# Optimization experiments

Measured on AMD Instinct MI355X. Metric: run time of the kernel, lower is better.

## Reference

```python
import jax, jax.numpy as jnp
import numpy as np

NUM_SKILLS = 1000
DIM_S = 64
SIZE_M = 64
B, T = 64, 200


def setup_inputs() -> dict:
    key = jax.random.key(0)
    ks = jax.random.split(key, 16)
    skills = jax.random.randint(ks[0], (B, T), 0, NUM_SKILLS)
    responses = jax.random.randint(ks[1], (B, T), 0, 2)
    s = 1.0 / np.sqrt(DIM_S)
    return {
        "skills": skills,
        "responses": responses,
        "k_emb": jax.random.normal(ks[2], (NUM_SKILLS, DIM_S)) * s,
        "v_emb": jax.random.normal(ks[3], (2 * NUM_SKILLS, DIM_S)) * s,
        "Mk": jax.random.normal(ks[4], (SIZE_M, DIM_S)) * np.sqrt(2.0 / DIM_S),
        "Mv0": jax.random.normal(ks[5], (SIZE_M, DIM_S)) * np.sqrt(2.0 / DIM_S),
        "fW": jax.random.normal(ks[6], (DIM_S, 2 * DIM_S)) * (1.0 / np.sqrt(2 * DIM_S)),
        "fb": jnp.zeros((DIM_S,)),
        "eW": jax.random.normal(ks[7], (DIM_S, DIM_S)) * s,
        "eb": jnp.zeros((DIM_S,)),
        "aW": jax.random.normal(ks[8], (DIM_S, DIM_S)) * s,
        "ab": jnp.zeros((DIM_S,)),
        "pW": jax.random.normal(ks[9], (1, DIM_S)) * s,
        "pb": jnp.zeros((1,)),
    }


def reference(skills, responses, k_emb, v_emb, Mk, Mv0, fW, fb, eW, eb, aW, ab, pW, pb):
    # dropout is identity in eval mode
    masked_r = responses * (responses > -1).astype(responses.dtype)
    x = skills + NUM_SKILLS * masked_r            # [B, T]
    k = k_emb[skills]                              # [B, T, D]
    v = v_emb[x]                                   # [B, T, D]
    w = jax.nn.softmax(jnp.einsum('btd,md->btm', k, Mk), axis=-1)  # [B, T, M]
    e = jax.nn.sigmoid(v @ eW.T + eb)              # [B, T, D]
    a = jnp.tanh(v @ aW.T + ab)                    # [B, T, D]

    Mv_init = jnp.broadcast_to(Mv0, (skills.shape[0],) + Mv0.shape)  # [B, M, D]

    def step(Mvt, inp):
        wt, et, at = inp                           # [B,M], [B,D], [B,D]
        read = jnp.einsum('bm,bmd->bd', wt, Mvt)   # read BEFORE update (Mv[:, :-1])
        Mvt = Mvt * (1.0 - wt[:, :, None] * et[:, None, :]) + wt[:, :, None] * at[:, None, :]
        return Mvt, read

    xs = (jnp.swapaxes(w, 0, 1), jnp.swapaxes(e, 0, 1), jnp.swapaxes(a, 0, 1))
    _, reads = jax.lax.scan(step, Mv_init, xs)     # reads: [T, B, D]
    reads = jnp.swapaxes(reads, 0, 1)              # [B, T, D]

    f = jnp.tanh(jnp.concatenate([reads, k], axis=-1) @ fW.T + fb)  # [B, T, D]
    p = jax.nn.sigmoid(f @ pW.T + pb)[..., 0]      # [B, T]
    return p[:, 1:]                                # pred, [B, T-1]
```

## Files before the change

### kernel.cpp

```cpp
#include <hip/hip_runtime.h>
#include <stdint.h>

#define NSK 1000
#define TT  200
#define BB  64
#define NROW (BB * TT)
#define NOUT (BB * (TT-1))
#define SCH 10
#define RW  2
#define NSPLIT 8
#define PSTR ((size_t)NROW * 64)

__device__ __forceinline__ unsigned ulane_bcast(unsigned v, int l) {
  return __builtin_amdgcn_readlane(v, l);
}
__device__ __forceinline__ float frcp(float x) { return __builtin_amdgcn_rcpf(x); }
__device__ __forceinline__ float sigm(float x) { return frcp(1.f + __expf(-x)); }
__device__ __forceinline__ float tanh_fast(float x) {
  return fmaf(-2.f, frcp(1.f + __expf(2.f * x)), 1.f);
}

typedef _Float16 half2v __attribute__((ext_vector_type(2)));
typedef _Float16 v8h __attribute__((ext_vector_type(8)));
typedef float    v4f __attribute__((ext_vector_type(4)));
union H2U { unsigned u; half2v h; };
union V8U { uint4 u; v8h h; };
__device__ __forceinline__ unsigned pack2h(float a, float b) {
  H2U x; x.h = (half2v){(_Float16)a, (_Float16)b}; return x.u;
}
__device__ __forceinline__ unsigned short f16bits(float x) {
  H2U u; u.h = (half2v){(_Float16)x, (_Float16)0.f}; return (unsigned short)(u.u & 0xffffu);
}
__device__ __forceinline__ float f16lo(unsigned bits) {
  H2U u; u.u = bits; return (float)u.h.x;
}
__device__ __forceinline__ float f16hi(unsigned bits) {
  H2U u; u.u = bits; return (float)u.h.y;
}
__device__ __forceinline__ v8h pk8(float4 x0, float4 x1) {
  return (v8h){(_Float16)x0.x, (_Float16)x0.y, (_Float16)x0.z, (_Float16)x0.w,
               (_Float16)x1.x, (_Float16)x1.y, (_Float16)x1.z, (_Float16)x1.w};
}

__global__ __launch_bounds__(256) void wea_scan(
    const int* __restrict__ skills, const int* __restrict__ responses,
    const float* __restrict__ k_emb, const float* __restrict__ v_emb,
    const float* __restrict__ Mk, const float* __restrict__ eW,
    const float* __restrict__ eb, const float* __restrict__ aW,
    const float* __restrict__ ab, const float* __restrict__ Mv0,
    unsigned short* __restrict__ pbase)
{
  __shared__ unsigned ea_lds[TT * 64];
  __shared__ unsigned short w_lds[TT * 8];
  __shared__ float red[2][SCH * 256];

  const int tid  = threadIdx.x;
  const int wv   = tid >> 6, lane = tid & 63;
  const int b    = blockIdx.x >> 3, s = blockIdx.x & 7;
  const int lr   = lane & 15;
  const int lg   = lane >> 4;
  const int cw   = s >> 1, lrh = s & 1;

  {
    float ebv[4], abv[4];
    #pragma unroll
    for (int c = 0; c < 4; ++c) { ebv[c] = eb[16 * c + lr]; abv[c] = ab[16 * c + lr]; }

    #pragma unroll 1
    for (int t = wv; t < 13; t += 4) {
      const int rbase = t * 16;
      const int rl    = min(rbase + lr, TT - 1);
      const int row   = b * TT + rl;
      const int sk = skills[row];
      int rr = responses[row]; rr = (rr > -1) ? rr : 0;
      const float4* kq = (const float4*)(k_emb + (size_t)sk * 64);
      const float4* vq = (const float4*)(v_emb + (size_t)(sk + NSK * rr) * 64);
      v8h ak[2], av[2];
      #pragma unroll
      for (int u = 0; u < 2; ++u) {
        const int o = u * 8 + lg * 2;
        ak[u] = pk8(kq[o], kq[o + 1]);
        av[u] = pk8(vq[o], vq[o + 1]);
      }

      v4f acK[4], acE[4], acA[4];
      #pragma unroll
      for (int c = 0; c < 4; ++c) {
        acK[c] = (v4f){0.f, 0.f, 0.f, 0.f};
        acE[c] = (v4f){0.f, 0.f, 0.f, 0.f};
        acA[c] = (v4f){0.f, 0.f, 0.f, 0.f};
      }
      #pragma unroll
      for (int c = 0; c < 4; ++c) {
        const float4* mq = (const float4*)(Mk + (size_t)(16 * c + lr) * 64);
        const float4* eq = (const float4*)(eW + (size_t)(16 * c + lr) * 64);
        const float4* aq = (const float4*)(aW + (size_t)(16 * c + lr) * 64);
        #pragma unroll
        for (int u = 0; u < 2; ++u) {
          const int o = u * 8 + lg * 2;
          const v8h bm = pk8(mq[o], mq[o + 1]);
          const v8h be = pk8(eq[o], eq[o + 1]);
          const v8h ba = pk8(aq[o], aq[o + 1]);
          acK[c] = __builtin_amdgcn_mfma_f32_16x16x32_f16(ak[u], bm, acK[c], 0, 0, 0);
          acE[c] = __builtin_amdgcn_mfma_f32_16x16x32_f16(av[u], be, acE[c], 0, 0, 0);
          acA[c] = __builtin_amdgcn_mfma_f32_16x16x32_f16(av[u], ba, acA[c], 0, 0, 0);
        }
      }

      float rs[4];
      #pragma unroll
      for (int q = 0; q < 4; ++q) {
        float m = fmaxf(fmaxf(acK[0][q], acK[1][q]), fmaxf(acK[2][q], acK[3][q]));
        #pragma unroll
        for (int off = 8; off; off >>= 1) m = fmaxf(m, __shfl_xor(m, off));
        float sm = 0.f;
        #pragma unroll
        for (int c = 0; c < 4; ++c) {
          acK[c][q] = __expf(acK[c][q] - m);
          sm += acK[c][q];
        }
        #pragma unroll
        for (int off = 8; off; off >>= 1) sm += __shfl_xor(sm, off);
        rs[q] = frcp(sm);
      }

      #pragma unroll
      for (int c = 0; c < 4; ++c) {
        const int j = 16 * c + lr;
        #pragma unroll
        for (int q = 0; q < 4; ++q) {
          const int rloc = rbase + lg * 4 + q;
          if (rloc < TT) {
            const float ev  = sigm(acE[c][q] + ebv[c]);
            const float avv = tanh_fast(acA[c][q] + abv[c]);
            ea_lds[rloc * 64 + j] = pack2h(ev, avv);
            if (c == cw && (lr >> 3) == lrh)
              w_lds[rloc * 8 + (lr & 7)] = f16bits(acK[c][q] * rs[q]);
          }
        }
      }
    }
  }
  __syncthreads();

  {
    const int m0 = s * 8 + wv * RW;
    unsigned short* ps = pbase + (size_t)s * PSTR;
    const size_t base = (size_t)b * TT;
    float Mv[RW];
    #pragma unroll
    for (int i = 0; i < RW; ++i) Mv[i] = Mv0[(size_t)(m0 + i) * 64 + lane];

    #pragma unroll 1
    for (int ch = 0; ch < TT / SCH; ++ch) {
      const int t0 = ch * SCH;
      float* rbuf = red[ch & 1];
      unsigned eab[SCH], wvb[SCH];
      #pragma unroll
      for (int k = 0; k < SCH; ++k) {
        eab[k] = ea_lds[(t0 + k) * 64 + lane];
        wvb[k] = (unsigned)w_lds[(t0 + k) * 8 + wv * RW + (lane & (RW - 1))];
      }
      #pragma unroll
      for (int k = 0; k < SCH; ++k) {
        const float ev = f16lo(eab[k]), av = f16hi(eab[k]);
        float rp = 0.f;
        #pragma unroll
        for (int i = 0; i < RW; ++i) {
          const float wm = f16lo(ulane_bcast(wvb[k], i));
          rp = fmaf(wm, Mv[i], rp);
          float tp = fmaf(-ev, Mv[i], av);
          Mv[i] = fmaf(wm, tp, Mv[i]);
        }
        rbuf[k * 256 + wv * 64 + lane] = rp;
      }
      __syncthreads();
      for (int k = wv; k < SCH; k += 4) {
        const float* rr2 = rbuf + k * 256;
        const float v = (rr2[lane] + rr2[64 + lane]) + (rr2[128 + lane] + rr2[192 + lane]);
        ps[(base + t0 + k) * 64 + lane] = f16bits(v);
      }
    }
  }
}

__global__ __launch_bounds__(256) void fp_mfma(
    const int* __restrict__ skills, const float* __restrict__ k_emb,
    const float* __restrict__ fW, const float* __restrict__ fb,
    const float* __restrict__ pW, const float* __restrict__ pb,
    const unsigned short* __restrict__ pbase,
    float* __restrict__ out)
{
  const int tid  = threadIdx.x;
  const int wv   = tid >> 6, lane = tid & 63;
  const int lr   = lane & 15;
  const int lg   = lane >> 4;
  const int o0   = (blockIdx.x * 4 + wv) * 16;

  const unsigned idx = o0 + lr;
  const unsigned bb  = idx / 199u;
  const unsigned t2  = idx - bb * 199u;
  const int srow     = (int)(idx + bb + 1u);

  v8h ar[4];
  #pragma unroll
  for (int t = 0; t < 2; ++t) {
    const size_t eo = (size_t)srow * 64 + t * 32 + lg * 8;
    V8U s0, s1, s2, s3;
    s0.u = *(const uint4*)&pbase[eo];
    s1.u = *(const uint4*)&pbase[eo + PSTR];
    s2.u = *(const uint4*)&pbase[eo + 2 * PSTR];
    s3.u = *(const uint4*)&pbase[eo + 3 * PSTR];
    v8h acc = (s0.h + s1.h) + (s2.h + s3.h);
    s0.u = *(const uint4*)&pbase[eo + 4 * PSTR];
    s1.u = *(const uint4*)&pbase[eo + 5 * PSTR];
    s2.u = *(const uint4*)&pbase[eo + 6 * PSTR];
    s3.u = *(const uint4*)&pbase[eo + 7 * PSTR];
    ar[t] = acc + ((s0.h + s1.h) + (s2.h + s3.h));
  }
  {
    const float4* kq = (const float4*)(k_emb + (size_t)skills[srow] * 64);
    #pragma unroll
    for (int t = 2; t < 4; ++t) {
      const int o = (t - 2) * 8 + lg * 2;
      ar[t] = pk8(kq[o], kq[o + 1]);
    }
  }

  float fbv[4], pwv[4];
  #pragma unroll
  for (int c = 0; c < 4; ++c) { fbv[c] = fb[16 * c + lr]; pwv[c] = pW[16 * c + lr]; }

  v4f acc[4];
  #pragma unroll
  for (int c = 0; c < 4; ++c) acc[c] = (v4f){0.f, 0.f, 0.f, 0.f};

  const float4* fq = (const float4*)fW;
  #pragma unroll
  for (int c = 0; c < 4; ++c) {
    const int jb = (16 * c + lr) * 32;
    #pragma unroll
    for (int t = 0; t < 4; ++t) {
      const int o = jb + t * 8 + lg * 2;
      const v8h bf = pk8(fq[o], fq[o + 1]);
      acc[c] = __builtin_amdgcn_mfma_f32_16x16x32_f16(ar[t], bf, acc[c], 0, 0, 0);
    }
  }

  const float pb0 = pb[0];
  #pragma unroll
  for (int q = 0; q < 4; ++q) {
    float s = 0.f;
    #pragma unroll
    for (int c = 0; c < 4; ++c)
      s += tanh_fast(acc[c][q] + fbv[c]) * pwv[c];
    #pragma unroll
    for (int off = 8; off; off >>= 1) s += __shfl_xor(s, off);
    if (lr == lg * 4 + q)
      out[(size_t)bb * (TT - 1) + t2] = sigm(s + pb0);
  }
}

extern "C" void kernel_launch(void* const* d_in, const int* in_sizes, int n_in,
                              void* d_out, int out_size, void* d_ws, size_t ws_size,
                              hipStream_t stream) {
  const int* skills    = (const int*)d_in[0];
  const int* responses = (const int*)d_in[1];
  const float* k_emb   = (const float*)d_in[2];
  const float* v_emb   = (const float*)d_in[3];
  const float* Mk      = (const float*)d_in[4];
  const float* Mv0     = (const float*)d_in[5];
  const float* fW      = (const float*)d_in[6];
  const float* fb      = (const float*)d_in[7];
  const float* eW      = (const float*)d_in[8];
  const float* eb      = (const float*)d_in[9];
  const float* aW      = (const float*)d_in[10];
  const float* ab      = (const float*)d_in[11];
  const float* pW      = (const float*)d_in[12];
  const float* pb      = (const float*)d_in[13];
  (void)in_sizes; (void)n_in; (void)out_size; (void)ws_size;

  unsigned short* pbase = (unsigned short*)d_ws;

  wea_scan<<<dim3(BB * NSPLIT), 256, 0, stream>>>(
      skills, responses, k_emb, v_emb, Mk, eW, eb, aW, ab, Mv0, pbase);
  fp_mfma<<<dim3(199), 256, 0, stream>>>(
      skills, k_emb, fW, fb, pW, pb, pbase, (float*)d_out);
}
```

Before: 132.2 us.

## Split scan across D columns instead of memory slots, removing partial-read reduction

Each of the 8 blocks per batch now owns 8 of the 64 D columns and all 64 memory slots, instead of 8 memory slots and all columns. The e/a projection therefore only computes its 16-column slice, and the read reduction over slots is done in-block with shuffles and a small LDS buffer. Each block writes final reads directly, so the second kernel no longer sums 8 fp16 partial buffers. The cost is shuffles every timestep and full 64-slot softmax weights kept in LDS; the scan chunk size also goes from 10 to 20.

Measured after the change: 137.1 us. +3.7%, slower.

```diff
diff --git a/kernel.cpp b/kernel.cpp
--- a/kernel.cpp
+++ b/kernel.cpp
@@ -5,15 +5,8 @@
 #define TT  200
 #define BB  64
 #define NROW (BB * TT)
-#define NOUT (BB * (TT-1))
-#define SCH 10
-#define RW  2
-#define NSPLIT 8
-#define PSTR ((size_t)NROW * 64)
-
-__device__ __forceinline__ unsigned ulane_bcast(unsigned v, int l) {
-  return __builtin_amdgcn_readlane(v, l);
-}
+#define SCH 20
+
 __device__ __forceinline__ float frcp(float x) { return __builtin_amdgcn_rcpf(x); }
 __device__ __forceinline__ float sigm(float x) { return frcp(1.f + __expf(-x)); }
 __device__ __forceinline__ float tanh_fast(float x) {
@@ -42,30 +35,27 @@
                (_Float16)x1.x, (_Float16)x1.y, (_Float16)x1.z, (_Float16)x1.w};
 }
 
-__global__ __launch_bounds__(256) void wea_scan(
+__global__ __launch_bounds__(256) void wea_scan_d(
     const int* __restrict__ skills, const int* __restrict__ responses,
     const float* __restrict__ k_emb, const float* __restrict__ v_emb,
     const float* __restrict__ Mk, const float* __restrict__ eW,
     const float* __restrict__ eb, const float* __restrict__ aW,
     const float* __restrict__ ab, const float* __restrict__ Mv0,
-    unsigned short* __restrict__ pbase)
+    unsigned short* __restrict__ reads_ws)
 {
-  __shared__ unsigned ea_lds[TT * 64];
-  __shared__ unsigned short w_lds[TT * 8];
-  __shared__ float red[2][SCH * 256];
+  __shared__ unsigned short w_lds[TT * 68];
+  __shared__ unsigned ea9[TT * 9];
+  __shared__ float red[2][SCH * 33];
 
   const int tid  = threadIdx.x;
   const int wv   = tid >> 6, lane = tid & 63;
-  const int b    = blockIdx.x >> 3, s = blockIdx.x & 7;
+  const int b    = blockIdx.x >> 3, q = blockIdx.x & 7;
+  const int cq   = q >> 1, h = q & 1;
   const int lr   = lane & 15;
   const int lg   = lane >> 4;
-  const int cw   = s >> 1, lrh = s & 1;
 
   {
-    float ebv[4], abv[4];
-    #pragma unroll
-    for (int c = 0; c < 4; ++c) { ebv[c] = eb[16 * c + lr]; abv[c] = ab[16 * c + lr]; }
-
+    const float ebl = eb[16 * cq + lr], abl = ab[16 * cq + lr];
     #pragma unroll 1
     for (int t = wv; t < 13; t += 4) {
       const int rbase = t * 16;
@@ -83,59 +73,63 @@
         av[u] = pk8(vq[o], vq[o + 1]);
       }
 
-      v4f acK[4], acE[4], acA[4];
-      #pragma unroll
-      for (int c = 0; c < 4; ++c) {
-        acK[c] = (v4f){0.f, 0.f, 0.f, 0.f};
-        acE[c] = (v4f){0.f, 0.f, 0.f, 0.f};
-        acA[c] = (v4f){0.f, 0.f, 0.f, 0.f};
-      }
+      v4f acK[4], acE, acA;
+      #pragma unroll
+      for (int c = 0; c < 4; ++c) acK[c] = (v4f){0.f, 0.f, 0.f, 0.f};
+      acE = (v4f){0.f, 0.f, 0.f, 0.f};
+      acA = (v4f){0.f, 0.f, 0.f, 0.f};
+
       #pragma unroll
       for (int c = 0; c < 4; ++c) {
         const float4* mq = (const float4*)(Mk + (size_t)(16 * c + lr) * 64);
-        const float4* eq = (const float4*)(eW + (size_t)(16 * c + lr) * 64);
-        const float4* aq = (const float4*)(aW + (size_t)(16 * c + lr) * 64);
         #pragma unroll
         for (int u = 0; u < 2; ++u) {
           const int o = u * 8 + lg * 2;
           const v8h bm = pk8(mq[o], mq[o + 1]);
+          acK[c] = __builtin_amdgcn_mfma_f32_16x16x32_f16(ak[u], bm, acK[c], 0, 0, 0);
+        }
+      }
+      {
+        const float4* eq = (const float4*)(eW + (size_t)(16 * cq + lr) * 64);
+        const float4* aq = (const float4*)(aW + (size_t)(16 * cq + lr) * 64);
+        #pragma unroll
+        for (int u = 0; u < 2; ++u) {
+          const int o = u * 8 + lg * 2;
           const v8h be = pk8(eq[o], eq[o + 1]);
           const v8h ba = pk8(aq[o], aq[o + 1]);
-          acK[c] = __builtin_amdgcn_mfma_f32_16x16x32_f16(ak[u], bm, acK[c], 0, 0, 0);
-          acE[c] = __builtin_amdgcn_mfma_f32_16x16x32_f16(av[u], be, acE[c], 0, 0, 0);
-          acA[c] = __builtin_amdgcn_mfma_f32_16x16x32_f16(av[u], ba, acA[c], 0, 0, 0);
+          acE = __builtin_amdgcn_mfma_f32_16x16x32_f16(av[u], be, acE, 0, 0, 0);
+          acA = __builtin_amdgcn_mfma_f32_16x16x32_f16(av[u], ba, acA, 0, 0, 0);
         }
       }
 
       float rs[4];
       #pragma unroll
-      for (int q = 0; q < 4; ++q) {
-        float m = fmaxf(fmaxf(acK[0][q], acK[1][q]), fmaxf(acK[2][q], acK[3][q]));
+      for (int p = 0; p < 4; ++p) {
+        float m = fmaxf(fmaxf(acK[0][p], acK[1][p]), fmaxf(acK[2][p], acK[3][p]));
         #pragma unroll
         for (int off = 8; off; off >>= 1) m = fmaxf(m, __shfl_xor(m, off));
         float sm = 0.f;
         #pragma unroll
         for (int c = 0; c < 4; ++c) {
-          acK[c][q] = __expf(acK[c][q] - m);
-          sm += acK[c][q];
+          acK[c][p] = __expf(acK[c][p] - m);
+          sm += acK[c][p];
         }
         #pragma unroll
         for (int off = 8; off; off >>= 1) sm += __shfl_xor(sm, off);
-        rs[q] = frcp(sm);
-      }
-
-      #pragma unroll
-      for (int c = 0; c < 4; ++c) {
-        const int j = 16 * c + lr;
-        #pragma unroll
-        for (int q = 0; q < 4; ++q) {
-          const int rloc = rbase + lg * 4 + q;
-          if (rloc < TT) {
-            const float ev  = sigm(acE[c][q] + ebv[c]);
-            const float avv = tanh_fast(acA[c][q] + abv[c]);
-            ea_lds[rloc * 64 + j] = pack2h(ev, avv);
-            if (c == cw && (lr >> 3) == lrh)
-              w_lds[rloc * 8 + (lr & 7)] = f16bits(acK[c][q] * rs[q]);
+        rs[p] = frcp(sm);
+      }
+
+      #pragma unroll
+      for (int p = 0; p < 4; ++p) {
+        const int rloc = rbase + lg * 4 + p;
+        if (rloc < TT) {
+          #pragma unroll
+          for (int c = 0; c < 4; ++c)
+            w_lds[rloc * 68 + 16 * c + lr] = f16bits(acK[c][p] * rs[p]);
+          if ((lr >> 3) == h) {
+            const float ev  = sigm(acE[p] + ebl);
+            const float avv = tanh_fast(acA[p] + abl);
+            ea9[rloc * 9 + (lr & 7)] = pack2h(ev, avv);
           }
         }
       }
@@ -144,41 +138,39 @@
   __syncthreads();
 
   {
-    const int m0 = s * 8 + wv * RW;
-    unsigned short* ps = pbase + (size_t)s * PSTR;
+    const int mg = lane & 7;
+    const int dl = lane >> 3;
+    const unsigned* w32 = (const unsigned*)w_lds;
     const size_t base = (size_t)b * TT;
-    float Mv[RW];
-    #pragma unroll
-    for (int i = 0; i < RW; ++i) Mv[i] = Mv0[(size_t)(m0 + i) * 64 + lane];
+
+    float Mva = Mv0[(size_t)(16 * wv + 2 * mg) * 64 + 8 * q + dl];
+    float Mvb = Mv0[(size_t)(16 * wv + 2 * mg + 1) * 64 + 8 * q + dl];
 
     #pragma unroll 1
     for (int ch = 0; ch < TT / SCH; ++ch) {
       const int t0 = ch * SCH;
       float* rbuf = red[ch & 1];
-      unsigned eab[SCH], wvb[SCH];
       #pragma unroll
       for (int k = 0; k < SCH; ++k) {
-        eab[k] = ea_lds[(t0 + k) * 64 + lane];
-        wvb[k] = (unsigned)w_lds[(t0 + k) * 8 + wv * RW + (lane & (RW - 1))];
-      }
-      #pragma unroll
-      for (int k = 0; k < SCH; ++k) {
-        const float ev = f16lo(eab[k]), av = f16hi(eab[k]);
-        float rp = 0.f;
-        #pragma unroll
-        for (int i = 0; i < RW; ++i) {
-          const float wm = f16lo(ulane_bcast(wvb[k], i));
-          rp = fmaf(wm, Mv[i], rp);
-          float tp = fmaf(-ev, Mv[i], av);
-          Mv[i] = fmaf(wm, tp, Mv[i]);
-        }
-        rbuf[k * 256 + wv * 64 + lane] = rp;
+        const int t = t0 + k;
+        const unsigned wpair = w32[t * 34 + 8 * wv + mg];
+        const unsigned eap   = ea9[t * 9 + dl];
+        const float w0 = f16lo(wpair), w1 = f16hi(wpair);
+        const float ev = f16lo(eap),   av = f16hi(eap);
+        float rp = fmaf(w1, Mvb, w0 * Mva);
+        Mva = fmaf(w0, fmaf(-ev, Mva, av), Mva);
+        Mvb = fmaf(w1, fmaf(-ev, Mvb, av), Mvb);
+        rp += __shfl_xor(rp, 1);
+        rp += __shfl_xor(rp, 2);
+        rp += __shfl_xor(rp, 4);
+        if (mg == 0) rbuf[k * 33 + wv * 8 + dl] = rp;
       }
       __syncthreads();
-      for (int k = wv; k < SCH; k += 4) {
-        const float* rr2 = rbuf + k * 256;
-        const float v = (rr2[lane] + rr2[64 + lane]) + (rr2[128 + lane] + rr2[192 + lane]);
-        ps[(base + t0 + k) * 64 + lane] = f16bits(v);
+      for (int idx = lane + 64 * wv; idx < SCH * 8; idx += 256) {
+        const int t = idx >> 3, d = idx & 7;
+        const float v = (rbuf[t * 33 + d]       + rbuf[t * 33 + 8 + d])
+                      + (rbuf[t * 33 + 16 + d]  + rbuf[t * 33 + 24 + d]);
+        reads_ws[(base + t0 + t) * 64 + 8 * q + d] = f16bits(v);
       }
     }
   }
@@ -188,7 +180,7 @@
     const int* __restrict__ skills, const float* __restrict__ k_emb,
     const float* __restrict__ fW, const float* __restrict__ fb,
     const float* __restrict__ pW, const float* __restrict__ pb,
-    const unsigned short* __restrict__ pbase,
+    const unsigned short* __restrict__ reads_ws,
     float* __restrict__ out)
 {
   const int tid  = threadIdx.x;
@@ -205,18 +197,9 @@
   v8h ar[4];
   #pragma unroll
   for (int t = 0; t < 2; ++t) {
-    const size_t eo = (size_t)srow * 64 + t * 32 + lg * 8;
-    V8U s0, s1, s2, s3;
-    s0.u = *(const uint4*)&pbase[eo];
-    s1.u = *(const uint4*)&pbase[eo + PSTR];
-    s2.u = *(const uint4*)&pbase[eo + 2 * PSTR];
-    s3.u = *(const uint4*)&pbase[eo + 3 * PSTR];
-    v8h acc = (s0.h + s1.h) + (s2.h + s3.h);
-    s0.u = *(const uint4*)&pbase[eo + 4 * PSTR];
-    s1.u = *(const uint4*)&pbase[eo + 5 * PSTR];
-    s2.u = *(const uint4*)&pbase[eo + 6 * PSTR];
-    s3.u = *(const uint4*)&pbase[eo + 7 * PSTR];
-    ar[t] = acc + ((s0.h + s1.h) + (s2.h + s3.h));
+    V8U s;
+    s.u = *(const uint4*)&reads_ws[(size_t)srow * 64 + t * 32 + lg * 8];
+    ar[t] = s.h;
   }
   {
     const float4* kq = (const float4*)(k_emb + (size_t)skills[srow] * 64);
@@ -249,14 +232,14 @@
 
   const float pb0 = pb[0];
   #pragma unroll
-  for (int q = 0; q < 4; ++q) {
+  for (int p = 0; p < 4; ++p) {
     float s = 0.f;
     #pragma unroll
     for (int c = 0; c < 4; ++c)
-      s += tanh_fast(acc[c][q] + fbv[c]) * pwv[c];
+      s += tanh_fast(acc[c][p] + fbv[c]) * pwv[c];
     #pragma unroll
     for (int off = 8; off; off >>= 1) s += __shfl_xor(s, off);
-    if (lr == lg * 4 + q)
+    if (lr == lg * 4 + p)
       out[(size_t)bb * (TT - 1) + t2] = sigm(s + pb0);
   }
 }
@@ -280,10 +263,10 @@
   const float* pb      = (const float*)d_in[13];
   (void)in_sizes; (void)n_in; (void)out_size; (void)ws_size;
 
-  unsigned short* pbase = (unsigned short*)d_ws;
-
-  wea_scan<<<dim3(BB * NSPLIT), 256, 0, stream>>>(
-      skills, responses, k_emb, v_emb, Mk, eW, eb, aW, ab, Mv0, pbase);
+  unsigned short* reads_ws = (unsigned short*)d_ws;
+
+  wea_scan_d<<<dim3(BB * 8), 256, 0, stream>>>(
+      skills, responses, k_emb, v_emb, Mk, eW, eb, aW, ab, Mv0, reads_ws);
   fp_mfma<<<dim3(199), 256, 0, stream>>>(
-      skills, k_emb, fW, fb, pW, pb, pbase, (float*)d_out);
-}
+      skills, k_emb, fW, fb, pW, pb, reads_ws, (float*)d_out);
+}
```
